# Kernel optimization log

Hardware: AMD Instinct MI355X
Metric: run time of the kernel (lower is better)

The kernel has to match this reference:

```python
import jax, jax.numpy as jnp
import numpy as np

N, S, D = 512, 64, 128   # num_nodes, seq_len, model_size
H, K = 4, 32             # num_heads, key_size
E = 4096                 # num_edges
WF = 4                   # widening_factor
EPS = 1e-5


def _alibi(num_heads, seq_len):
    slopes = 2.0 ** (-8.0 * (jnp.arange(1, num_heads + 1, dtype=jnp.float32) / num_heads))
    pos = jnp.arange(seq_len, dtype=jnp.float32)
    rel = pos[None, :] - pos[:, None]  # T - t, <= 0 in causal region
    return (slopes[:, None, None] * rel)[None]  # [1,H,S,S]


def layer_norm(x, scale, offset):
    mu = jnp.mean(x, axis=-1, keepdims=True)
    var = jnp.var(x, axis=-1, keepdims=True)
    return (x - mu) * jax.lax.rsqrt(var + EPS) * scale + offset


def segment_softmax(logits, seg, num_segments):
    maxs = jax.ops.segment_max(logits, seg, num_segments=num_segments)
    e = jnp.exp(logits - maxs[seg])
    denom = jax.ops.segment_sum(e, seg, num_segments=num_segments)
    return e / denom[seg]


def setup_inputs() -> dict:
    key = jax.random.key(0)
    ks = jax.random.split(key, 24)
    sd = 0.02
    inp = {
        'nodes': jax.random.normal(ks[0], (N, S, D), jnp.float32),
        'senders': jax.random.randint(ks[1], (E,), 0, N, jnp.int32),
        'receivers': jax.random.randint(ks[2], (E,), 0, N, jnp.int32),
        'alibi_mask': _alibi(H, S),
        'ln1_s': jnp.ones((D,)), 'ln1_b': jnp.zeros((D,)),
        'wq': jax.random.normal(ks[3], (D, H * K)) * sd, 'bq': jnp.zeros((H * K,)),
        'wk': jax.random.normal(ks[4], (D, H * K)) * sd, 'bk': jnp.zeros((H * K,)),
        'wv': jax.random.normal(ks[5], (D, H * K)) * sd, 'bv': jnp.zeros((H * K,)),
        'wo': jax.random.normal(ks[6], (H * K, D)) * sd, 'bo': jnp.zeros((D,)),
        'ln2_s': jnp.ones((D,)), 'ln2_b': jnp.zeros((D,)),
        'w1': jax.random.normal(ks[7], (D, WF * D)) * sd, 'b1': jnp.zeros((WF * D,)),
        'w2': jax.random.normal(ks[8], (WF * D, D)) * sd, 'b2': jnp.zeros((D,)),
        'ln3_s': jnp.ones((D,)), 'ln3_b': jnp.zeros((D,)),
        'w_sa': jax.random.normal(ks[9], (2 * D, D)) * sd, 'b_sa': jnp.zeros((D,)),
        'w_sq': jax.random.normal(ks[10], (D, H * D)) * sd, 'b_sq': jnp.zeros((H * D,)),
    }
    return inp


def reference(nodes, senders, receivers, alibi_mask,
              ln1_s, ln1_b, wq, bq, wk, bk, wv, bv, wo, bo,
              ln2_s, ln2_b, w1, b1, w2, b2, ln3_s, ln3_b,
              w_sa, b_sa, w_sq, b_sq):
    n, s, d = nodes.shape
    # --- node self-attention with ALiBi + causal mask ---
    xn = layer_norm(nodes, ln1_s, ln1_b)
    q = (xn @ wq + bq).reshape(n, s, H, K)
    k = (xn @ wk + bk).reshape(n, s, H, K)
    v = (xn @ wv + bv).reshape(n, s, H, K)
    logits = jnp.einsum('nthk,nThk->nhtT', q, k)
    logits = alibi_mask + logits / jnp.sqrt(jnp.float32(K))
    causal = jnp.tril(jnp.ones((1, 1, s, s), dtype=bool))
    logits = jnp.where(causal, logits, -1e30)
    w = jax.nn.softmax(logits, axis=-1)
    attn = jnp.einsum('nhtT,nThk->nthk', w, v).reshape(n, s, H * K)
    nodes = nodes + (attn @ wo + bo)  # dropout rate 0 (eval)
    # --- FFN block ---
    xn = layer_norm(nodes, ln2_s, ln2_b)
    dense = jax.nn.gelu(xn @ w1 + b1) @ w2 + b2
    nodes = layer_norm(nodes + dense, ln3_s, ln3_b)
    # --- graph message passing: gather / segment-softmax / segment-sum ---
    sent = nodes[senders]        # [E,S,D]
    recv = nodes[receivers]      # [E,S,D]
    sl = jnp.concatenate([sent, recv], axis=-1) @ w_sa + b_sa  # [E,S,D]
    aw = segment_softmax(sl, receivers, n)                     # [E,S,D]
    sq = (aw @ w_sq + b_sq).reshape(E, s, H, d)                # [E,S,H,D]
    messages = jnp.mean(sq * sent[:, :, None, :], axis=2)      # [E,S,D]
    out = jax.ops.segment_sum(messages, receivers, num_segments=n)
    return out
```

## Files before the change

kernel.cpp:

```cpp
#include <hip/hip_runtime.h>
#include <hip/hip_bf16.h>

typedef __hip_bfloat16 bf16;
typedef __attribute__((ext_vector_type(8))) __bf16 bf8v;
typedef __attribute__((ext_vector_type(4))) float  f4v;

#define NN 512
#define SSEQ 64
#define DDIM 128
#define HH 4
#define NROWS (NN*SSEQ)
#define EMAX 4096
#define ECH 64

__device__ __forceinline__ float b2f(bf16 x){ return __bfloat162float(x); }
__device__ __forceinline__ bf16 f2b(float x){ return __float2bfloat16(x); }
__device__ __forceinline__ float ldf(float x){ return x; }
__device__ __forceinline__ float ldf(bf16 x){ return b2f(x); }
__device__ __forceinline__ void stf(float* p, float v){ *p = v; }
__device__ __forceinline__ void stf(bf16* p, float v){ *p = f2b(v); }

__device__ __forceinline__ f4v mfma16(bf8v a, bf8v b, f4v c){
  return __builtin_amdgcn_mfma_f32_16x16x32_bf16(a, b, c, 0, 0, 0);
}
__device__ __forceinline__ bf8v ldfrag(const void* p){
  return __builtin_bit_cast(bf8v, *(const int4*)p);
}
__device__ __forceinline__ float gelu_f(float v){
  return 0.5f*v*(1.0f + tanhf(0.7978845608028654f*(v + 0.044715f*v*v*v)));
}

__global__ __launch_bounds__(512) void prep_all_k(
    const float* wq, const float* wk, const float* wv, const float* wo,
    const float* w1, const float* w2, const float* wsa,
    const float* w_sq, const float* b_sq,
    const float* bq, const float* bk, const float* bv,
    const int* __restrict__ receivers,
    bf16* wqkvT, bf16* woT, bf16* w1T, bf16* w2T, bf16* wsaTt,
    bf16* wbarT, float* bbar, float* qkv_bias,
    int* off, int* perm, int* chunk_cnt, int E){
  int b = blockIdx.x, t = threadIdx.x;
  if (b < 832){
    if (t >= 256) return;
    const float* W; bf16* Wt; int K, lN, rel, roff = 0;
    if      (b < 64) { W=wq;  Wt=wqkvT; K=128; lN=7; rel=b;     roff=0;   }
    else if (b <128) { W=wk;  Wt=wqkvT; K=128; lN=7; rel=b-64;  roff=128; }
    else if (b <192) { W=wv;  Wt=wqkvT; K=128; lN=7; rel=b-128; roff=256; }
    else if (b <256) { W=wo;  Wt=woT;   K=128; lN=7; rel=b-192; }
    else if (b <512) { W=w1;  Wt=w1T;   K=128; lN=9; rel=b-256; }
    else if (b <768) { W=w2;  Wt=w2T;   K=512; lN=7; rel=b-512; }
    else             { W=wsa; Wt=wsaTt; K=128; lN=7; rel=b-768; }
    int i = rel*256 + t;
    int k = i >> lN, n = i & ((1<<lN)-1);
    Wt[(size_t)(n+roff)*K + k] = f2b(W[i]);
  } else if (b < 896){
    if (t >= 256) return;
    int i = (b-832)*256 + t;
    int c = i>>7, d = i&127;
    float s = 0.f;
    #pragma unroll
    for (int h=0;h<HH;++h) s += w_sq[(size_t)c*(HH*DDIM) + h*DDIM + d];
    wbarT[d*DDIM + c] = f2b(0.25f*s);
  } else if (b < 898){
    if (t >= 256) return;
    int idx = (b-896)*256 + t;
    if (idx < 128){
      float s = 0.f;
      #pragma unroll
      for (int h=0;h<HH;++h) s += b_sq[h*DDIM + idx];
      bbar[idx] = 0.25f*s;
    } else if (idx < 512){
      int j = idx - 128;
      float v = (j<128) ? bq[j] : (j<256) ? bk[j-128] : bv[j-256];
      qkv_bias[j] = v;
    }
  } else if (b == 898){
    __shared__ int s_cnt[NN];
    s_cnt[t] = 0;
    __syncthreads();
    for (int e=t; e<E; e+=512) atomicAdd(&s_cnt[receivers[e]], 1);
    __syncthreads();
    int deg = s_cnt[t];
    int acc = 0, myrank = 0;
    for (int i=0;i<NN;++i){
      int di = s_cnt[i];
      acc    += (i<t) ? di : 0;
      myrank += ((di > deg) || (di == deg && i < t)) ? 1 : 0;
    }
    off[t] = acc;
    if (t==NN-1) off[NN] = acc + deg;
    perm[myrank] = t;
  } else {
    __shared__ int hc[NN];
    int c = b - 899;
    for (int i=t;i<NN;i+=512) hc[i]=0;
    __syncthreads();
    if (t < ECH){
      int e = c*ECH + t;
      if (e < E) atomicAdd(&hc[receivers[e]], 1);
    }
    __syncthreads();
    for (int i=t;i<NN;i+=512) chunk_cnt[(size_t)c*NN + i] = hc[i];
  }
}

__global__ __launch_bounds__(512) void base_k(const int* __restrict__ off,
    const int* __restrict__ chunk_cnt, int* __restrict__ base, int nch){
  int n = threadIdx.x;
  int run = off[n];
  for (int c=0;c<nch;++c){
    base[(size_t)c*NN + n] = run;
    run += chunk_cnt[(size_t)c*NN + n];
  }
}

__global__ __launch_bounds__(64) void slot_k(const int* __restrict__ senders,
    const int* __restrict__ receivers, const int* __restrict__ base,
    int* __restrict__ slot_snd, int E){
  int t = threadIdx.x, c = blockIdx.x;
  int e = c*ECH + t;
  bool valid = (e < E);
  int r  = valid ? receivers[e] : -1;
  int sd = valid ? senders[e]   : 0;
  int rank = 0;
  #pragma unroll
  for (int i=0;i<64;++i){
    int ri = __shfl(r, i);
    rank += (i < t && ri == r) ? 1 : 0;
  }
  if (valid) slot_snd[base[(size_t)c*NN + r] + rank] = sd;
}

template<typename TIN, typename TOUT>
__global__ __launch_bounds__(256) void ln_k(const TIN* __restrict__ x,
    const float* __restrict__ sc, const float* __restrict__ of,
    TOUT* __restrict__ y){
  int row  = blockIdx.x*4 + (threadIdx.x>>6);
  int lane = threadIdx.x & 63;
  size_t base = (size_t)row*DDIM;
  float v0 = ldf(x[base+lane]);
  float v1 = ldf(x[base+lane+64]);
  float s = v0+v1, q = v0*v0+v1*v1;
  #pragma unroll
  for (int m=1;m<64;m<<=1){ s += __shfl_xor(s,m); q += __shfl_xor(q,m); }
  float mu   = s*(1.0f/DDIM);
  float var  = q*(1.0f/DDIM) - mu*mu;
  float rstd = rsqrtf(var + 1e-5f);
  stf(&y[base+lane],    (v0-mu)*rstd*sc[lane]    + of[lane]);
  stf(&y[base+lane+64], (v1-mu)*rstd*sc[lane+64] + of[lane+64]);
}

template<int KT, int ACT, typename TR, bool RES, bool BIAS>
__global__ __launch_bounds__(256) void gemm_m(const bf16* __restrict__ A,
    const bf16* __restrict__ Wt, const float* __restrict__ bias,
    const TR* __restrict__ R, bf16* __restrict__ C, int N){
  __shared__ bf16 sA[64][72];
  __shared__ bf16 sB[64][72];
  int t = threadIdx.x;
  int bm = blockIdx.x, bn = blockIdx.y;
  int w = t>>6, lane = t&63;
  int wr = w>>1, wc = w&1;
  f4v acc[2][2] = {};
  for (int ks=0; ks<KT; ks+=64){
    #pragma unroll
    for (int p=0;p<2;++p){
      int r = p*32 + (t>>3), cc = (t&7)*8;
      *(int4*)(&sA[r][cc]) = *(const int4*)(A  + (size_t)(bm*64+r)*KT + ks + cc);
      *(int4*)(&sB[r][cc]) = *(const int4*)(Wt + (size_t)(bn*64+r)*KT + ks + cc);
    }
    __syncthreads();
    #pragma unroll
    for (int k0=0;k0<64;k0+=32){
      int kc = k0 + 8*(lane>>4);
      bf8v a0 = ldfrag(&sA[wr*32      + (lane&15)][kc]);
      bf8v a1 = ldfrag(&sA[wr*32 + 16 + (lane&15)][kc]);
      bf8v b0 = ldfrag(&sB[wc*32      + (lane&15)][kc]);
      bf8v b1 = ldfrag(&sB[wc*32 + 16 + (lane&15)][kc]);
      acc[0][0] = mfma16(a0, b0, acc[0][0]);
      acc[0][1] = mfma16(a0, b1, acc[0][1]);
      acc[1][0] = mfma16(a1, b0, acc[1][0]);
      acc[1][1] = mfma16(a1, b1, acc[1][1]);
    }
    __syncthreads();
  }
  #pragma unroll
  for (int j=0;j<2;++j){
    int gcol = bn*64 + wc*32 + j*16 + (lane&15);
    float bs = BIAS ? bias[gcol] : 0.f;
    #pragma unroll
    for (int i=0;i<2;++i){
      #pragma unroll
      for (int r=0;r<4;++r){
        int grow = bm*64 + wr*32 + i*16 + 4*(lane>>4) + r;
        float v = acc[i][j][r] + bs;
        if (ACT==1) v = gelu_f(v);
        if (ACT==2) v = __expf(v);
        if (RES) v += ldf(R[(size_t)grow*N + gcol]);
        C[(size_t)grow*N + gcol] = f2b(v);
      }
    }
  }
}

__global__ __launch_bounds__(256) void gemm_wo_ln2_k(const bf16* __restrict__ A,
    const bf16* __restrict__ Wt, const float* __restrict__ bias,
    const float* __restrict__ Rres, const float* __restrict__ lns,
    const float* __restrict__ lnb, bf16* __restrict__ n2out,
    bf16* __restrict__ xnout){
  __shared__ bf16 sA[64][72];
  __shared__ bf16 sB[128][72];
  __shared__ float s_st[2][2][32][2];
  int t = threadIdx.x, bm = blockIdx.x;
  int w = t>>6, lane = t&63, ls = lane&15, lg = lane>>4;
  int wr = w>>1, wc = w&1;
  f4v acc[2][4] = {};
  for (int ks=0; ks<128; ks+=64){
    #pragma unroll
    for (int p=0;p<2;++p){
      int r = p*32 + (t>>3), cc = (t&7)*8;
      *(int4*)(&sA[r][cc]) = *(const int4*)(A + (size_t)(bm*64+r)*128 + ks + cc);
    }
    #pragma unroll
    for (int p=0;p<4;++p){
      int r = p*32 + (t>>3), cc = (t&7)*8;
      *(int4*)(&sB[r][cc]) = *(const int4*)(Wt + (size_t)r*128 + ks + cc);
    }
    __syncthreads();
    #pragma unroll
    for (int k0=0;k0<64;k0+=32){
      int kc = k0 + 8*lg;
      bf8v a0 = ldfrag(&sA[wr*32      + ls][kc]);
      bf8v a1 = ldfrag(&sA[wr*32 + 16 + ls][kc]);
      #pragma unroll
      for (int j=0;j<4;++j){
        bf8v bj = ldfrag(&sB[wc*64 + j*16 + ls][kc]);
        acc[0][j] = mfma16(a0, bj, acc[0][j]);
        acc[1][j] = mfma16(a1, bj, acc[1][j]);
      }
    }
    __syncthreads();
  }
  float x[2][4][4];
  float psum[2][4], psq[2][4];
  #pragma unroll
  for (int i=0;i<2;++i)
    #pragma unroll
    for (int r=0;r<4;++r){ psum[i][r]=0.f; psq[i][r]=0.f; }
  #pragma unroll
  for (int i=0;i<2;++i){
    #pragma unroll
    for (int j=0;j<4;++j){
      int col = wc*64 + j*16 + ls;
      float bs = bias[col];
      #pragma unroll
      for (int r=0;r<4;++r){
        int row = bm*64 + wr*32 + i*16 + 4*lg + r;
        float v = acc[i][j][r] + bs + Rres[(size_t)row*128 + col];
        x[i][j][r] = v;
        psum[i][r] += v;
        psq[i][r]  += v*v;
        n2out[(size_t)row*128 + col] = f2b(v);
      }
    }
  }
  #pragma unroll
  for (int i=0;i<2;++i)
    #pragma unroll
    for (int r=0;r<4;++r){
      float s_=psum[i][r], q_=psq[i][r];
      s_ += __shfl_xor(s_,1); s_ += __shfl_xor(s_,2);
      s_ += __shfl_xor(s_,4); s_ += __shfl_xor(s_,8);
      q_ += __shfl_xor(q_,1); q_ += __shfl_xor(q_,2);
      q_ += __shfl_xor(q_,4); q_ += __shfl_xor(q_,8);
      if (ls == 0){
        int rl = i*16 + 4*lg + r;
        s_st[wr][wc][rl][0] = s_;
        s_st[wr][wc][rl][1] = q_;
      }
    }
  __syncthreads();
  #pragma unroll
  for (int i=0;i<2;++i){
    #pragma unroll
    for (int r=0;r<4;++r){
      int rl = i*16 + 4*lg + r;
      float s_ = s_st[wr][0][rl][0] + s_st[wr][1][rl][0];
      float q_ = s_st[wr][0][rl][1] + s_st[wr][1][rl][1];
      float mu = s_*(1.0f/DDIM);
      float var = q_*(1.0f/DDIM) - mu*mu;
      float rstd = rsqrtf(var + 1e-5f);
      int row = bm*64 + wr*32 + rl;
      #pragma unroll
      for (int j=0;j<4;++j){
        int col = wc*64 + j*16 + ls;
        xnout[(size_t)row*128 + col] = f2b((x[i][j][r]-mu)*rstd*lns[col] + lnb[col]);
      }
    }
  }
}

__global__ __launch_bounds__(256) void gemm_w2_tail_k(const bf16* __restrict__ A,
    const bf16* __restrict__ Wt, const float* __restrict__ bias,
    const bf16* __restrict__ Rres, const float* __restrict__ lns,
    const float* __restrict__ lnb, const bf16* __restrict__ wsaT,
    bf16* __restrict__ r2out, bf16* __restrict__ yexpout){
  __shared__ bf16 sA[64][72];
  __shared__ bf16 sB[128][72];
  __shared__ bf16 sY[64][136];
  __shared__ float s_st[2][2][32][2];
  int t = threadIdx.x, bm = blockIdx.x;
  int w = t>>6, lane = t&63, ls = lane&15, lg = lane>>4;
  int wr = w>>1, wc = w&1;
  f4v acc[2][4] = {};
  for (int ks=0; ks<512; ks+=64){
    #pragma unroll
    for (int p=0;p<2;++p){
      int r = p*32 + (t>>3), cc = (t&7)*8;
      *(int4*)(&sA[r][cc]) = *(const int4*)(A + (size_t)(bm*64+r)*512 + ks + cc);
    }
    #pragma unroll
    for (int p=0;p<4;++p){
      int r = p*32 + (t>>3), cc = (t&7)*8;
      *(int4*)(&sB[r][cc]) = *(const int4*)(Wt + (size_t)r*512 + ks + cc);
    }
    __syncthreads();
    #pragma unroll
    for (int k0=0;k0<64;k0+=32){
      int kc = k0 + 8*lg;
      bf8v a0 = ldfrag(&sA[wr*32      + ls][kc]);
      bf8v a1 = ldfrag(&sA[wr*32 + 16 + ls][kc]);
      #pragma unroll
      for (int j=0;j<4;++j){
        bf8v bj = ldfrag(&sB[wc*64 + j*16 + ls][kc]);
        acc[0][j] = mfma16(a0, bj, acc[0][j]);
        acc[1][j] = mfma16(a1, bj, acc[1][j]);
      }
    }
    __syncthreads();
  }
  float x[2][4][4];
  float psum[2][4], psq[2][4];
  #pragma unroll
  for (int i=0;i<2;++i)
    #pragma unroll
    for (int r=0;r<4;++r){ psum[i][r]=0.f; psq[i][r]=0.f; }
  #pragma unroll
  for (int i=0;i<2;++i){
    #pragma unroll
    for (int j=0;j<4;++j){
      int col = wc*64 + j*16 + ls;
      float bs = bias[col];
      #pragma unroll
      for (int r=0;r<4;++r){
        int row = bm*64 + wr*32 + i*16 + 4*lg + r;
        float v = acc[i][j][r] + bs + b2f(Rres[(size_t)row*128 + col]);
        x[i][j][r] = v;
        psum[i][r] += v;
        psq[i][r]  += v*v;
      }
    }
  }
  #pragma unroll
  for (int i=0;i<2;++i)
    #pragma unroll
    for (int r=0;r<4;++r){
      float s_=psum[i][r], q_=psq[i][r];
      s_ += __shfl_xor(s_,1); s_ += __shfl_xor(s_,2);
      s_ += __shfl_xor(s_,4); s_ += __shfl_xor(s_,8);
      q_ += __shfl_xor(q_,1); q_ += __shfl_xor(q_,2);
      q_ += __shfl_xor(q_,4); q_ += __shfl_xor(q_,8);
      if (ls == 0){
        int rl = i*16 + 4*lg + r;
        s_st[wr][wc][rl][0] = s_;
        s_st[wr][wc][rl][1] = q_;
      }
    }
  __syncthreads();
  #pragma unroll
  for (int i=0;i<2;++i){
    #pragma unroll
    for (int r=0;r<4;++r){
      int rl = i*16 + 4*lg + r;
      float s_ = s_st[wr][0][rl][0] + s_st[wr][1][rl][0];
      float q_ = s_st[wr][0][rl][1] + s_st[wr][1][rl][1];
      float mu = s_*(1.0f/DDIM);
      float var = q_*(1.0f/DDIM) - mu*mu;
      float rstd = rsqrtf(var + 1e-5f);
      int row = bm*64 + wr*32 + rl;
      #pragma unroll
      for (int j=0;j<4;++j){
        int col = wc*64 + j*16 + ls;
        bf16 yb = f2b((x[i][j][r]-mu)*rstd*lns[col] + lnb[col]);
        r2out[(size_t)row*128 + col] = yb;
        sY[wr*32 + rl][col] = yb;
      }
    }
  }
  __syncthreads();
  f4v acc2[2][4] = {};
  for (int ks2=0; ks2<128; ks2+=64){
    #pragma unroll
    for (int p=0;p<4;++p){
      int r = p*32 + (t>>3), cc = (t&7)*8;
      *(int4*)(&sB[r][cc]) = *(const int4*)(wsaT + (size_t)r*128 + ks2 + cc);
    }
    __syncthreads();
    #pragma unroll
    for (int k0=0;k0<64;k0+=32){
      int kc = k0 + 8*lg;
      bf8v a0 = ldfrag(&sY[wr*32      + ls][ks2 + kc]);
      bf8v a1 = ldfrag(&sY[wr*32 + 16 + ls][ks2 + kc]);
      #pragma unroll
      for (int j=0;j<4;++j){
        bf8v bj = ldfrag(&sB[wc*64 + j*16 + ls][kc]);
        acc2[0][j] = mfma16(a0, bj, acc2[0][j]);
        acc2[1][j] = mfma16(a1, bj, acc2[1][j]);
      }
    }
    __syncthreads();
  }
  #pragma unroll
  for (int i=0;i<2;++i){
    #pragma unroll
    for (int j=0;j<4;++j){
      int col = wc*64 + j*16 + ls;
      #pragma unroll
      for (int r=0;r<4;++r){
        int row = bm*64 + wr*32 + i*16 + 4*lg + r;
        yexpout[(size_t)row*128 + col] = f2b(__expf(acc2[i][j][r]));
      }
    }
  }
}

__global__ __launch_bounds__(256) void attn_m(const bf16* __restrict__ qkvb,
    bf16* __restrict__ ob){
  __shared__ bf16 sVT[128][72];
  __shared__ bf16 sP[4][64][72];
  int t = threadIdx.x, n = blockIdx.x;
  int w = t>>6, lane = t&63, ls = lane&15, lg = lane>>4;
  const bf16* qbase = qkvb + (size_t)n*SSEQ*(3*DDIM);
  bf8v qf[4], kf[4];
  #pragma unroll
  for (int mi=0;mi<4;++mi)
    qf[mi] = ldfrag(qbase + (size_t)(16*mi + ls)*(3*DDIM) + 32*w + 8*lg);
  #pragma unroll
  for (int ni=0;ni<4;++ni)
    kf[ni] = ldfrag(qbase + (size_t)(16*ni + ls)*(3*DDIM) + DDIM + 32*w + 8*lg);
  for (int id = t; id < 1024; id += 256){
    int T = id>>4, c = id&15;
    int4 v = *(const int4*)(qbase + (size_t)T*(3*DDIM) + 2*DDIM + c*8);
    const bf16* pv = (const bf16*)&v;
    #pragma unroll
    for (int j=0;j<8;++j){
      int d = c*8 + j;
      sVT[d][T ^ (((d>>3)&7)<<3)] = pv[j];
    }
  }
  f4v accS[4][4];
  #pragma unroll
  for (int mi=0;mi<4;++mi)
    #pragma unroll
    for (int ni=0;ni<4;++ni){
      f4v z = {};
      accS[mi][ni] = mfma16(qf[mi], kf[ni], z);
    }
  __syncthreads();
  const float scale = 0.17677669529663687f;
  const float slope = 1.0f / (float)(4 << (2*w));
  float den[4][4];
  #pragma unroll
  for (int mi=0;mi<4;++mi)
    #pragma unroll
    for (int r=0;r<4;++r) den[mi][r] = 0.f;
  #pragma unroll
  for (int mi=0;mi<4;++mi){
    #pragma unroll
    for (int ni=0;ni<4;++ni){
      #pragma unroll
      for (int r=0;r<4;++r){
        int rel = (16*ni + ls) - (16*mi + 4*lg + r);
        float p = (rel <= 0) ? __expf(accS[mi][ni][r]*scale + slope*(float)rel) : 0.f;
        accS[mi][ni][r] = p;
        den[mi][r] += p;
      }
    }
  }
  #pragma unroll
  for (int mi=0;mi<4;++mi)
    #pragma unroll
    for (int r=0;r<4;++r){
      float d_ = den[mi][r];
      d_ += __shfl_xor(d_, 1);  d_ += __shfl_xor(d_, 2);
      d_ += __shfl_xor(d_, 4);  d_ += __shfl_xor(d_, 8);
      den[mi][r] = 1.0f / d_;
    }
  #pragma unroll
  for (int mi=0;mi<4;++mi)
    #pragma unroll
    for (int ni=0;ni<4;++ni)
      #pragma unroll
      for (int r=0;r<4;++r)
        sP[w][16*mi + 4*lg + r][16*ni + ls] = f2b(accS[mi][ni][r]*den[mi][r]);
  f4v oacc[4][2] = {};
  #pragma unroll
  for (int ks=0;ks<2;++ks){
    bf8v vf[2];
    #pragma unroll
    for (int ni2=0;ni2<2;++ni2){
      int d = 32*w + 16*ni2 + ls;
      vf[ni2] = ldfrag(&sVT[d][(32*ks + 8*lg) ^ (((d>>3)&7)<<3)]);
    }
    #pragma unroll
    for (int mi=0;mi<4;++mi){
      bf8v pa = ldfrag(&sP[w][16*mi + ls][32*ks + 8*lg]);
      #pragma unroll
      for (int ni2=0;ni2<2;++ni2)
        oacc[mi][ni2] = mfma16(pa, vf[ni2], oacc[mi][ni2]);
    }
  }
  #pragma unroll
  for (int mi=0;mi<4;++mi)
    #pragma unroll
    for (int ni2=0;ni2<2;++ni2)
      #pragma unroll
      for (int r=0;r<4;++r)
        ob[(size_t)(n*SSEQ + 16*mi + 4*lg + r)*DDIM + 32*w + 16*ni2 + ls]
          = f2b(oacc[mi][ni2][r]);
}

__global__ __launch_bounds__(256) void msg4_k(const bf16* __restrict__ yexp,
    const bf16* __restrict__ nodes3, const int* __restrict__ off,
    const int* __restrict__ slot_snd, const int* __restrict__ perm,
    const bf16* __restrict__ wbarT, const float* __restrict__ bbar,
    float* __restrict__ out){
  __shared__ bf16 sP[2][16][136];
  __shared__ bf16 s_sent[4][3][16][36];
  int t = threadIdx.x, sc = blockIdx.y;
  int n = perm[blockIdx.x];
  int w = t>>6, lane = t&63, ls = lane&15, lg = lane>>4;
  int off0 = off[n], deg = off[n+1]-off0;
  int dbase = w*32;
  if (deg == 0){
    #pragma unroll
    for (int ct=0;ct<2;++ct)
      #pragma unroll
      for (int r=0;r<4;++r)
        out[((size_t)n*SSEQ + sc*16 + 4*lg + r)*DDIM + dbase + ct*16 + ls] = 0.f;
    return;
  }
  bf8v B[2][4];
  #pragma unroll
  for (int ct=0;ct<2;++ct)
    #pragma unroll
    for (int kb=0;kb<4;++kb)
      B[ct][kb] = ldfrag(wbarT + (size_t)(dbase + ct*16 + ls)*DDIM + kb*32 + lg*8);
  float bb[2];
  #pragma unroll
  for (int ct=0;ct<2;++ct) bb[ct] = bbar[dbase + ct*16 + ls];
  int rp = t>>4, cp = (t&15)*8;
  size_t prow = ((size_t)(sc*16 + rp))*DDIM + cp;
  float den8[8];
  #pragma unroll
  for (int j=0;j<8;++j) den8[j] = 0.f;
  {
    int k = 0;
    for (; k+2<=deg; k+=2){
      int s0 = slot_snd[off0+k], s1 = slot_snd[off0+k+1];
      int4 v0 = *(const int4*)(yexp + (size_t)s0*SSEQ*DDIM + prow);
      int4 v1 = *(const int4*)(yexp + (size_t)s1*SSEQ*DDIM + prow);
      const bf16* a = (const bf16*)&v0;
      const bf16* b = (const bf16*)&v1;
      #pragma unroll
      for (int j=0;j<8;++j) den8[j] += b2f(a[j]) + b2f(b[j]);
    }
    if (k < deg){
      int s0 = slot_snd[off0+k];
      int4 v = *(const int4*)(yexp + (size_t)s0*SSEQ*DDIM + prow);
      const bf16* a = (const bf16*)&v;
      #pragma unroll
      for (int j=0;j<8;++j) den8[j] += b2f(a[j]);
    }
  }
  #pragma unroll
  for (int j=0;j<8;++j) den8[j] = 1.0f/den8[j];
  int rs = lane>>2, cs = (lane&3)*8;
  int4 yvP[1]; int4 yv1;
  {
    int snd = slot_snd[off0];
    int4 v = *(const int4*)(yexp + (size_t)snd*SSEQ*DDIM + prow);
    const bf16* a = (const bf16*)&v;
    bf16 pv[8];
    #pragma unroll
    for (int j=0;j<8;++j) pv[j] = f2b(b2f(a[j]) * den8[j]);
    *(int4*)&sP[0][rp][cp] = *(const int4*)pv;
    *(int4*)&s_sent[w][0][rs][cs] =
      *(const int4*)(nodes3 + ((size_t)snd*SSEQ + sc*16 + rs)*DDIM + dbase + cs);
  }
  if (deg > 1){
    int snd = slot_snd[off0+1];
    yv1 = *(const int4*)(yexp + (size_t)snd*SSEQ*DDIM + prow);
    *(int4*)&s_sent[w][1][rs][cs] =
      *(const int4*)(nodes3 + ((size_t)snd*SSEQ + sc*16 + rs)*DDIM + dbase + cs);
  }
  __syncthreads();
  f4v oacc[2] = {};
  int4 yvN;
  for (int k=0;k<deg;++k){
    int buf = k&1;
    if (k+2 < deg){
      int snd2 = slot_snd[off0+k+2];
      yvN = *(const int4*)(yexp + (size_t)snd2*SSEQ*DDIM + prow);
      *(int4*)&s_sent[w][(k+2)%3][rs][cs] =
        *(const int4*)(nodes3 + ((size_t)snd2*SSEQ + sc*16 + rs)*DDIM + dbase + cs);
    }
    if (k+1 < deg){
      const bf16* a = (const bf16*)&yv1;
      bf16 pv[8];
      #pragma unroll
      for (int j=0;j<8;++j) pv[j] = f2b(b2f(a[j]) * den8[j]);
      *(int4*)&sP[buf^1][rp][cp] = *(const int4*)pv;
    }
    bf8v a4[4];
    #pragma unroll
    for (int kb=0;kb<4;++kb) a4[kb] = ldfrag(&sP[buf][ls][kb*32 + lg*8]);
    f4v g[2] = {};
    #pragma unroll
    for (int kb=0;kb<4;++kb)
      #pragma unroll
      for (int ct=0;ct<2;++ct)
        g[ct] = mfma16(a4[kb], B[ct][kb], g[ct]);
    #pragma unroll
    for (int ct=0;ct<2;++ct)
      #pragma unroll
      for (int r=0;r<4;++r){
        float sent = b2f(s_sent[w][k%3][4*lg + r][ct*16 + ls]);
        oacc[ct][r] += (g[ct][r] + bb[ct]) * sent;
      }
    __syncthreads();
    yv1 = yvN;
  }
  #pragma unroll
  for (int ct=0;ct<2;++ct)
    #pragma unroll
    for (int r=0;r<4;++r)
      out[((size_t)n*SSEQ + sc*16 + 4*lg + r)*DDIM + dbase + ct*16 + ls] = oacc[ct][r];
}

extern "C" void kernel_launch(void* const* d_in, const int* in_sizes, int n_in,
                              void* d_out, int out_size, void* d_ws, size_t ws_size,
                              hipStream_t stream){
  const float* nodes = (const float*)d_in[0];
  const int*  senders   = (const int*)d_in[1];
  const int*  receivers = (const int*)d_in[2];
  const float* ln1_s=(const float*)d_in[4];  const float* ln1_b=(const float*)d_in[5];
  const float* wq=(const float*)d_in[6];     const float* bq=(const float*)d_in[7];
  const float* wk=(const float*)d_in[8];     const float* bk=(const float*)d_in[9];
  const float* wv=(const float*)d_in[10];    const float* bv_=(const float*)d_in[11];
  const float* wo=(const float*)d_in[12];    const float* bo=(const float*)d_in[13];
  const float* ln2_s=(const float*)d_in[14]; const float* ln2_b=(const float*)d_in[15];
  const float* w1=(const float*)d_in[16];    const float* b1=(const float*)d_in[17];
  const float* w2=(const float*)d_in[18];    const float* b2=(const float*)d_in[19];
  const float* ln3_s=(const float*)d_in[20]; const float* ln3_b=(const float*)d_in[21];
  const float* w_sa=(const float*)d_in[22];
  const float* w_sq=(const float*)d_in[24];  const float* b_sq=(const float*)d_in[25];
  int E = in_sizes[1];
  int nch = (E + ECH - 1)/ECH;

  const size_t MB = 1024*1024;
  char* ws = (char*)d_ws;
  bf16* xn      = (bf16*)(ws);
  bf16* qkvb    = (bf16*)(ws +  8*MB);
  bf16* n2      = (bf16*)(ws + 32*MB);
  bf16* xn2     = (bf16*)(ws + 48*MB);
  bf16* hb      = (bf16*)(ws);
  bf16* attnout = xn;
  bf16* r2     = (bf16*)(ws + 64*MB);
  bf16* yexp   = (bf16*)(ws + 72*MB);
  char* tail = ws + 88*MB;
  bf16*  wbarT   = (bf16*)tail;                       tail += DDIM*DDIM*2;
  float* bbar    = (float*)tail;                      tail += DDIM*4 + 512;
  float* qkv_bias= (float*)tail;                      tail += 3*DDIM*4;
  int*   off     = (int*)tail;                        tail += (NN+8)*4;
  int*   slot_snd= (int*)tail;                        tail += EMAX*4;
  int*   perm    = (int*)tail;                        tail += NN*4;
  int*   ccnt    = (int*)tail;                        tail += 64*NN*4;
  int*   cbase   = (int*)tail;                        tail += 64*NN*4;
  bf16*  wqkvT   = (bf16*)tail;                       tail += 384*128*2;
  bf16*  woT     = (bf16*)tail;                       tail += 128*128*2;
  bf16*  w1T     = (bf16*)tail;                       tail += 128*512*2;
  bf16*  w2T     = (bf16*)tail;                       tail += 512*128*2;
  bf16*  wsaTt   = (bf16*)tail;                       tail += 128*128*2;

  prep_all_k<<<899+nch,512,0,stream>>>(wq,wk,wv,wo,w1,w2,w_sa,w_sq,b_sq,bq,bk,bv_,
                                       receivers,
                                       wqkvT,woT,w1T,w2T,wsaTt,wbarT,bbar,qkv_bias,
                                       off, perm, ccnt, E);
  base_k<<<1,512,0,stream>>>(off, ccnt, cbase, nch);
  slot_k<<<nch,64,0,stream>>>(senders, receivers, cbase, slot_snd, E);

  ln_k<float,bf16><<<NROWS/4,256,0,stream>>>(nodes, ln1_s, ln1_b, xn);
  gemm_m<128,0,float,false,true><<<dim3(NROWS/64,6),256,0,stream>>>(xn, wqkvT, qkv_bias, (const float*)nullptr, qkvb, 384);
  attn_m<<<NN,256,0,stream>>>(qkvb, attnout);
  gemm_wo_ln2_k<<<NROWS/64,256,0,stream>>>(attnout, woT, bo, nodes, ln2_s, ln2_b, n2, xn2);
  gemm_m<128,1,bf16,false,true><<<dim3(NROWS/64,8),256,0,stream>>>(xn2, w1T, b1, (const bf16*)nullptr, hb, 512);
  gemm_w2_tail_k<<<NROWS/64,256,0,stream>>>(hb, w2T, b2, n2, ln3_s, ln3_b, wsaTt, r2, yexp);

  msg4_k<<<dim3(NN,4),256,0,stream>>>(yexp, r2, off, slot_snd, perm, wbarT, bbar, (float*)d_out);
}
```

Before: 152.4 us.

## Fuse LayerNorm1 into QKV GEMM and fold base scan into slot kernel

Replaces the separate LayerNorm kernel and QKV GEMM with one kernel. Each block normalizes its 64 rows into shared memory and loops over all six output column tiles, which removes the bf16 xn round trip through global memory and one launch. The base_k prefix kernel is also dropped: slot_k now sums the chunk counts for its receiver directly, removing a serial launch in exchange for redundant per-thread loops over chunks. The fused GEMM has fewer blocks (512 instead of 3072) and each block loops serially over its column tiles, which may reduce parallelism.

```diff
diff --git a/kernel.cpp b/kernel.cpp
--- a/kernel.cpp
+++ b/kernel.cpp
@@ -104,50 +104,101 @@
   }
 }
 
-__global__ __launch_bounds__(512) void base_k(const int* __restrict__ off,
-    const int* __restrict__ chunk_cnt, int* __restrict__ base, int nch){
-  int n = threadIdx.x;
-  int run = off[n];
-  for (int c=0;c<nch;++c){
-    base[(size_t)c*NN + n] = run;
-    run += chunk_cnt[(size_t)c*NN + n];
-  }
-}
-
 __global__ __launch_bounds__(64) void slot_k(const int* __restrict__ senders,
-    const int* __restrict__ receivers, const int* __restrict__ base,
-    int* __restrict__ slot_snd, int E){
+    const int* __restrict__ receivers, const int* __restrict__ off,
+    const int* __restrict__ chunk_cnt, int* __restrict__ slot_snd, int E){
   int t = threadIdx.x, c = blockIdx.x;
   int e = c*ECH + t;
   bool valid = (e < E);
   int r  = valid ? receivers[e] : -1;
   int sd = valid ? senders[e]   : 0;
+  int base = 0;
+  if (valid){
+    base = off[r];
+    for (int cp=0; cp<c; ++cp) base += chunk_cnt[(size_t)cp*NN + r];
+  }
   int rank = 0;
   #pragma unroll
   for (int i=0;i<64;++i){
     int ri = __shfl(r, i);
     rank += (i < t && ri == r) ? 1 : 0;
   }
-  if (valid) slot_snd[base[(size_t)c*NN + r] + rank] = sd;
-}
-
-template<typename TIN, typename TOUT>
-__global__ __launch_bounds__(256) void ln_k(const TIN* __restrict__ x,
-    const float* __restrict__ sc, const float* __restrict__ of,
-    TOUT* __restrict__ y){
-  int row  = blockIdx.x*4 + (threadIdx.x>>6);
-  int lane = threadIdx.x & 63;
-  size_t base = (size_t)row*DDIM;
-  float v0 = ldf(x[base+lane]);
-  float v1 = ldf(x[base+lane+64]);
-  float s = v0+v1, q = v0*v0+v1*v1;
-  #pragma unroll
-  for (int m=1;m<64;m<<=1){ s += __shfl_xor(s,m); q += __shfl_xor(q,m); }
-  float mu   = s*(1.0f/DDIM);
-  float var  = q*(1.0f/DDIM) - mu*mu;
-  float rstd = rsqrtf(var + 1e-5f);
-  stf(&y[base+lane],    (v0-mu)*rstd*sc[lane]    + of[lane]);
-  stf(&y[base+lane+64], (v1-mu)*rstd*sc[lane+64] + of[lane+64]);
+  if (valid) slot_snd[base + rank] = sd;
+}
+
+__global__ __launch_bounds__(256) void gemm_ln1qkv_k(const float* __restrict__ X,
+    const float* __restrict__ lns, const float* __restrict__ lnb,
+    const bf16* __restrict__ Wt, const float* __restrict__ bias,
+    bf16* __restrict__ C){
+  __shared__ bf16 sA[64][136];
+  __shared__ bf16 sB[64][72];
+  int t = threadIdx.x, bm = blockIdx.x;
+  int w = t>>6, lane = t&63, ls = lane&15, lg = lane>>4;
+  int wr = w>>1, wc = w&1;
+  {
+    int r = t>>2, q = t&3;
+    float vals[32];
+    const float* xr = X + (size_t)(bm*64 + r)*DDIM + q*32;
+    #pragma unroll
+    for (int p=0;p<8;++p){
+      float4 v = *(const float4*)(xr + p*4);
+      vals[p*4+0]=v.x; vals[p*4+1]=v.y; vals[p*4+2]=v.z; vals[p*4+3]=v.w;
+    }
+    float s=0.f, sq=0.f;
+    #pragma unroll
+    for (int j=0;j<32;++j){ s += vals[j]; sq += vals[j]*vals[j]; }
+    s  += __shfl_xor(s, 1);  s  += __shfl_xor(s, 2);
+    sq += __shfl_xor(sq, 1); sq += __shfl_xor(sq, 2);
+    float mu   = s*(1.0f/DDIM);
+    float var  = sq*(1.0f/DDIM) - mu*mu;
+    float rstd = rsqrtf(var + 1e-5f);
+    #pragma unroll
+    for (int p=0;p<4;++p){
+      bf16 pv[8];
+      #pragma unroll
+      for (int j=0;j<8;++j){
+        int cidx = q*32 + p*8 + j;
+        pv[j] = f2b((vals[p*8+j]-mu)*rstd*lns[cidx] + lnb[cidx]);
+      }
+      *(int4*)(&sA[r][q*32 + p*8]) = *(const int4*)pv;
+    }
+  }
+  for (int bn=0; bn<6; ++bn){
+    f4v acc[2][2] = {};
+    for (int ks=0; ks<128; ks+=64){
+      __syncthreads();
+      #pragma unroll
+      for (int p=0;p<2;++p){
+        int r = p*32 + (t>>3), cc = (t&7)*8;
+        *(int4*)(&sB[r][cc]) = *(const int4*)(Wt + (size_t)(bn*64+r)*128 + ks + cc);
+      }
+      __syncthreads();
+      #pragma unroll
+      for (int k0=0;k0<64;k0+=32){
+        int kc = ks + k0 + 8*lg;
+        bf8v a0 = ldfrag(&sA[wr*32      + ls][kc]);
+        bf8v a1 = ldfrag(&sA[wr*32 + 16 + ls][kc]);
+        bf8v b0 = ldfrag(&sB[wc*32      + ls][k0 + 8*lg]);
+        bf8v b1 = ldfrag(&sB[wc*32 + 16 + ls][k0 + 8*lg]);
+        acc[0][0] = mfma16(a0, b0, acc[0][0]);
+        acc[0][1] = mfma16(a0, b1, acc[0][1]);
+        acc[1][0] = mfma16(a1, b0, acc[1][0]);
+        acc[1][1] = mfma16(a1, b1, acc[1][1]);
+      }
+    }
+    #pragma unroll
+    for (int j=0;j<2;++j){
+      int gcol = bn*64 + wc*32 + j*16 + ls;
+      float bs = bias[gcol];
+      #pragma unroll
+      for (int i=0;i<2;++i)
+        #pragma unroll
+        for (int r=0;r<4;++r){
+          int grow = bm*64 + wr*32 + i*16 + 4*lg + r;
+          C[(size_t)grow*384 + gcol] = f2b(acc[i][j][r] + bs);
+        }
+    }
+  }
 }
 
 template<int KT, int ACT, typename TR, bool RES, bool BIAS>
@@ -585,7 +636,7 @@
   #pragma unroll
   for (int j=0;j<8;++j) den8[j] = 1.0f/den8[j];
   int rs = lane>>2, cs = (lane&3)*8;
-  int4 yvP[1]; int4 yv1;
+  int4 yv1;
   {
     int snd = slot_snd[off0];
     int4 v = *(const int4*)(yexp + (size_t)snd*SSEQ*DDIM + prow);
@@ -669,12 +720,11 @@
 
   const size_t MB = 1024*1024;
   char* ws = (char*)d_ws;
-  bf16* xn      = (bf16*)(ws);
+  bf16* attnout = (bf16*)(ws);
   bf16* qkvb    = (bf16*)(ws +  8*MB);
   bf16* n2      = (bf16*)(ws + 32*MB);
   bf16* xn2     = (bf16*)(ws + 48*MB);
   bf16* hb      = (bf16*)(ws);
-  bf16* attnout = xn;
   bf16* r2     = (bf16*)(ws + 64*MB);
   bf16* yexp   = (bf16*)(ws + 72*MB);
   char* tail = ws + 88*MB;
@@ -685,7 +735,6 @@
   int*   slot_snd= (int*)tail;                        tail += EMAX*4;
   int*   perm    = (int*)tail;                        tail += NN*4;
   int*   ccnt    = (int*)tail;                        tail += 64*NN*4;
-  int*   cbase   = (int*)tail;                        tail += 64*NN*4;
   bf16*  wqkvT   = (bf16*)tail;                       tail += 384*128*2;
   bf16*  woT     = (bf16*)tail;                       tail += 128*128*2;
   bf16*  w1T     = (bf16*)tail;                       tail += 128*512*2;
@@ -696,11 +745,9 @@
                                        receivers,
                                        wqkvT,woT,w1T,w2T,wsaTt,wbarT,bbar,qkv_bias,
                                        off, perm, ccnt, E);
-  base_k<<<1,512,0,stream>>>(off, ccnt, cbase, nch);
-  slot_k<<<nch,64,0,stream>>>(senders, receivers, cbase, slot_snd, E);
-
-  ln_k<float,bf16><<<NROWS/4,256,0,stream>>>(nodes, ln1_s, ln1_b, xn);
-  gemm_m<128,0,float,false,true><<<dim3(NROWS/64,6),256,0,stream>>>(xn, wqkvT, qkv_bias, (const float*)nullptr, qkvb, 384);
+  slot_k<<<nch,64,0,stream>>>(senders, receivers, off, ccnt, slot_snd, E);
+
+  gemm_ln1qkv_k<<<NROWS/64,256,0,stream>>>(nodes, ln1_s, ln1_b, wqkvT, qkv_bias, qkvb);
   attn_m<<<NN,256,0,stream>>>(qkvb, attnout);
   gemm_wo_ln2_k<<<NROWS/64,256,0,stream>>>(attnout, woT, bo, nodes, ln2_s, ln2_b, n2, xn2);
   gemm_m<128,1,bf16,false,true><<<dim3(NROWS/64,8),256,0,stream>>>(xn2, w1T, b1, (const bf16*)nullptr, hb, 512);
```

After: 145.1 us. 4.7% less time.
